# Kernel tuning notes

Hardware: AMD Instinct MI355X
Metric: run time of the kernel (lower is better)

The kernel has to match this reference:

```python
import jax, jax.numpy as jnp
import numpy as np


def _hard_sigmoid(x):
    # Keras ConvLSTM2D default recurrent_activation
    return jnp.clip(0.2 * x + 0.5, 0.0, 1.0)


def _conv(x, w):
    # NHWC input, HWIO kernel, SAME padding, stride 1
    return jax.lax.conv_general_dilated(
        x, w, (1, 1), 'SAME', dimension_numbers=('NHWC', 'HWIO', 'NHWC'))


def _convlstm(seq, h, c, k, rk, b):
    # seq: [B, T, H, W, Cin]; h, c: [B, H, W, F]
    # k: [kh, kw, Cin, 4F], rk: [kh, kw, F, 4F], b: [4F]
    def step(carry, x):
        h, c = carry
        z = _conv(x, k) + _conv(h, rk) + b  # [B,H,W,4F]
        zi, zf, zc, zo = jnp.split(z, 4, axis=-1)
        i = _hard_sigmoid(zi)
        f = _hard_sigmoid(zf)
        o = _hard_sigmoid(zo)
        c = f * c + i * jnp.tanh(zc)
        h = o * jnp.tanh(c)
        return (h, c), None
    (h, c), _ = jax.lax.scan(step, (h, c), jnp.swapaxes(seq, 0, 1))
    return h, c


def setup_inputs() -> dict:
    key = jax.random.key(0)
    ks = jax.random.split(key, 14)
    B, T, H, W, Cin, F, K = 32, 1, 64, 64, 1, 64, 3
    s = 0.05
    inp = {
        'input_': jax.random.normal(ks[0], (B, T, H, W, Cin), jnp.float32),
        'h0': jax.random.normal(ks[1], (B, H, W, F), jnp.float32) * s,
        'c0': jax.random.normal(ks[2], (B, H, W, F), jnp.float32) * s,
        'h1': jax.random.normal(ks[3], (B, H, W, F), jnp.float32) * s,
        'c1': jax.random.normal(ks[4], (B, H, W, F), jnp.float32) * s,
        'k0': jax.random.normal(ks[5], (K, K, Cin, 4 * F), jnp.float32) * s,
        'rk0': jax.random.normal(ks[6], (K, K, F, 4 * F), jnp.float32) * s,
        'b0': jnp.zeros((4 * F,), jnp.float32),
        'k1': jax.random.normal(ks[7], (K, K, F, 4 * F), jnp.float32) * s,
        'rk1': jax.random.normal(ks[8], (K, K, F, 4 * F), jnp.float32) * s,
        'b1': jnp.zeros((4 * F,), jnp.float32),
        'cw': jax.random.normal(ks[9], (1, 1, F, 1), jnp.float32) * s,
        'cb': jnp.zeros((1,), jnp.float32),
    }
    return inp


def reference(input_, h0, c0, h1, c1, k0, rk0, b0, k1, rk1, b1, cw, cb):
    # Layer 0 consumes the input frame sequence (T=1)
    h0n, c0n = _convlstm(input_, h0, c0, k0, rk0, b0)
    # Layer 1 consumes layer-0's last hidden state as its (length-1) input
    h1n, c1n = _convlstm(h0n[:, None], h1, c1, k1, rk1, b1)
    frames = _conv(h1n, cw) + cb  # 1x1 conv head -> [B,H,W,1]
    return frames, h0n, c0n, h1n, c1n
```

## Files before the change

kernel.cpp:

```cpp
#include <hip/hip_runtime.h>
#include <hip/hip_bf16.h>

typedef short s16;
typedef __attribute__((ext_vector_type(8))) short bf16x8;
typedef __attribute__((ext_vector_type(4))) float f32x4;

__device__ __forceinline__ s16 f2bf(float f) {
  unsigned u = __builtin_bit_cast(unsigned, f);
  unsigned r = (u + 0x7FFFu + ((u >> 16) & 1u)) >> 16;
  return (s16)r;
}

__device__ __forceinline__ float hsig(float x) {
  return fminf(fmaxf(0.2f * x + 0.5f, 0.0f), 1.0f);
}

#define PXS 66
#define ROWSZ (PXS * 64)
#define ASZ4 (4 * ROWSZ)

__global__ void wprep_kernel(const float* __restrict__ rk0, const float* __restrict__ k1,
                             const float* __restrict__ rk1, const float* __restrict__ k0,
                             s16* __restrict__ w0q, s16* __restrict__ w1q,
                             s16* __restrict__ w2q, s16* __restrict__ k0t) {
  int idx = blockIdx.x * 256 + threadIdx.x;
  const int n1 = 18 * 8192;
  if (idx < 3 * n1) {
    int which = idx / n1;
    int i = idx - which * n1;
    int e    = i & 7;
    int lane = (i >> 3) & 63;
    int g    = (i >> 9) & 3;
    int j    = (i >> 11) & 3;
    int k    = (i >> 13) & 1;
    int tap  = i >> 14;
    int l15 = lane & 15, l4 = lane >> 4;
    int ic = k * 32 + l4 * 8 + e;
    int oc = j * 64 + g * 16 + l15;
    const float* src = (which == 0) ? rk0 : (which == 1) ? k1 : rk1;
    s16* dst = (which == 0) ? w0q : (which == 1) ? w1q : w2q;
    dst[i] = f2bf(src[(tap * 64 + ic) * 256 + oc]);
  } else if (idx < 3 * n1 + 8192) {
    int r = idx - 3 * n1;
    int kk = r & 31;
    int oc = r >> 5;
    k0t[r] = (kk < 9) ? f2bf(k0[kk * 256 + oc]) : (s16)0;
  }
}

template <bool F32>
__device__ __forceinline__ bf16x8 load_conv8(const void* src, long off) {
  if constexpr (F32) {
    const float* p = (const float*)src + off;
    float4 v0 = *reinterpret_cast<const float4*>(p);
    float4 v1 = *reinterpret_cast<const float4*>(p + 4);
    bf16x8 r;
    r[0] = f2bf(v0.x); r[1] = f2bf(v0.y); r[2] = f2bf(v0.z); r[3] = f2bf(v0.w);
    r[4] = f2bf(v1.x); r[5] = f2bf(v1.y); r[6] = f2bf(v1.z); r[7] = f2bf(v1.w);
    return r;
  } else {
    return *reinterpret_cast<const bf16x8*>((const s16*)src + off);
  }
}

template <bool F32>
__device__ __forceinline__ void stage4(s16* a_lds, const void* src, int b, int y0, int tid) {
  #pragma unroll
  for (int i = 0; i < 2; ++i) {
    int c   = tid + i * 1024;
    int row = c >> 9;
    int px  = (c >> 3) & 63;
    int cb  = c & 7;
    int y   = y0 - 1 + row;
    int xp  = px + 1;
    bf16x8 v = {};
    if ((unsigned)y < 64u)
      v = load_conv8<F32>(src, ((long)(b * 64 + y) * 64 + px) * 64 + cb * 8);
    *reinterpret_cast<bf16x8*>(a_lds + (row * PXS + xp) * 64 + ((cb ^ (xp & 7)) * 8)) = v;
  }
  if (tid < 64) {
    int row = tid >> 4;
    int xp  = ((tid >> 3) & 1) ? 65 : 0;
    int cb  = tid & 7;
    bf16x8 z = {};
    *reinterpret_cast<bf16x8*>(a_lds + (row * PXS + xp) * 64 + cb * 8) = z;
  }
}

template <int NSRC, bool XPATH, bool S0F32, bool S1F32>
__global__ __launch_bounds__(1024, 4) void cell_kernel(
    const void* __restrict__ src0,
    const void* __restrict__ src1,
    const s16* __restrict__ w0,
    const s16* __restrict__ w1,
    const float* __restrict__ xin,
    const s16* __restrict__ k0t,
    const float* __restrict__ bias,
    const float* __restrict__ c_old,
    float* __restrict__ h_out,
    float* __restrict__ c_out,
    s16* __restrict__ hb_out)
{
  __shared__ __align__(16) s16 a_lds[NSRC * ASZ4];
  __shared__ __align__(16) s16 w_lds[4][8192];
  __shared__ float x_lds[XPATH ? 256 : 1];

  const int tid = threadIdx.x;
  const int b  = blockIdx.x >> 5;
  const int y0 = (blockIdx.x & 31) << 1;

  const int wave = tid >> 6;
  const int lane = tid & 63;
  const int g    = wave & 3;
  const int mq   = wave >> 2;
  const int l15  = lane & 15;
  const int l4   = lane >> 4;

  constexpr int NST = NSRC * 18;

  auto issueW = [&](int u) {
    int v = (u >= NST) ? u - NST : u;
    int si = (NSRC == 2 && v >= 18) ? 1 : 0;
    int vv = v - 18 * si;
    const s16* wt = (si ? w1 : w0) + vv * 8192;
    char* base = (char*)(&w_lds[0][0]) + (u & 3) * 16384 + (tid >> 6) * 1024;
    __builtin_amdgcn_global_load_lds(
        (const __attribute__((address_space(1))) void*)(wt + tid * 8),
        (__attribute__((address_space(3))) void*)base, 16, 0, 0);
  };

  auto readWf = [&](bf16x8 (&wf)[4], int u) {
    const s16* wb = &w_lds[u & 3][0] + g * 512 + lane * 8;
    #pragma unroll
    for (int j = 0; j < 4; ++j)
      wf[j] = *reinterpret_cast<const bf16x8*>(wb + j * 2048);
  };

  auto readA = [&](bf16x8 (&af)[2], int u) {
    int v = (u >= NST) ? u - NST : u;
    int si = (NSRC == 2 && v >= 18) ? 1 : 0;
    int uu = v - 18 * si;
    int tap = uu >> 1, kk = uu & 1;
    int dy = tap / 3, dx = tap - dy * 3;
    const char* sb = (const char*)a_lds + si * (ASZ4 * 2) + ((mq >> 1) + dy) * (ROWSZ * 2);
    #pragma unroll
    for (int m = 0; m < 2; ++m) {
      int xq   = (mq & 1) * 32 + m * 16 + l15 + dx;
      int boff = xq * 128 + ((((kk << 2) | l4) ^ (xq & 7)) << 4);
      af[m] = *reinterpret_cast<const bf16x8*>(sb + boff);
    }
  };

  f32x4 acc[2][4] = {};

  auto doMfma = [&](const bf16x8 (&af)[2], const bf16x8 (&wf)[4]) {
    __builtin_amdgcn_s_setprio(1);
    #pragma unroll
    for (int m = 0; m < 2; ++m) {
      #pragma unroll
      for (int j = 0; j < 4; ++j)
        acc[m][j] = __builtin_amdgcn_mfma_f32_16x16x32_bf16(af[m], wf[j], acc[m][j], 0, 0, 0);
    }
    __builtin_amdgcn_s_setprio(0);
  };

  issueW(0);
  issueW(1);
  issueW(2);
  stage4<S0F32>(a_lds, src0, b, y0, tid);
  if (NSRC == 2) stage4<S1F32>(a_lds + ASZ4, src1, b, y0, tid);
  if (XPATH) {
    if (tid < 256) {
      int row = tid >> 6, px = tid & 63;
      int y = y0 - 1 + row;
      x_lds[tid] = ((unsigned)y < 64u) ? xin[(b * 64 + y) * 64 + px] : 0.0f;
    }
  }
  __syncthreads();

  if (XPATH) {
    const int rb = mq >> 1;
    #pragma unroll
    for (int m = 0; m < 2; ++m) {
      int px = (mq & 1) * 32 + m * 16 + l15;
      bf16x8 ax = {};
      #pragma unroll
      for (int e = 0; e < 8; ++e) {
        int t = l4 * 8 + e;
        if (t < 9) {
          int dyt = t / 3, dxt = t - dyt * 3;
          int xx = px + dxt - 1;
          float xv = ((unsigned)xx < 64u) ? x_lds[(rb + dyt) * 64 + xx] : 0.0f;
          ax[e] = f2bf(xv);
        }
      }
      #pragma unroll
      for (int j = 0; j < 4; ++j) {
        int oc = j * 64 + g * 16 + l15;
        bf16x8 bx = *reinterpret_cast<const bf16x8*>(k0t + oc * 32 + l4 * 8);
        acc[m][j] = __builtin_amdgcn_mfma_f32_16x16x32_bf16(ax, bx, acc[m][j], 0, 0, 0);
      }
    }
  }

  bf16x8 afA[2], afB[2], wfA[4], wfB[4];
  readA(afA, 0);
  readWf(wfA, 0);
  #pragma unroll
  for (int u = 0; u < NST; u += 2) {
    asm volatile("s_waitcnt vmcnt(1)" ::: "memory");
    __builtin_amdgcn_s_barrier();
    issueW(u + 3);
    readA(afB, u + 1);
    readWf(wfB, u + 1);
    doMfma(afA, wfA);
    asm volatile("s_waitcnt vmcnt(1)" ::: "memory");
    __builtin_amdgcn_s_barrier();
    issueW(u + 4);
    readA(afA, u + 2);
    readWf(wfA, u + 2);
    doMfma(afB, wfB);
  }

  float bi[4];
  #pragma unroll
  for (int j = 0; j < 4; ++j) bi[j] = bias[j * 64 + g * 16 + l15];

  const int pix_base = b * 4096 + y0 * 64;
  const int f = g * 16 + l15;
  #pragma unroll
  for (int m = 0; m < 2; ++m) {
    #pragma unroll
    for (int r = 0; r < 4; ++r) {
      int pl = mq * 32 + m * 16 + l4 * 4 + r;
      int off = (pix_base + pl) * 64 + f;
      float zi = acc[m][0][r] + bi[0];
      float zf = acc[m][1][r] + bi[1];
      float zc = acc[m][2][r] + bi[2];
      float zo = acc[m][3][r] + bi[3];
      float ig = hsig(zi), fg = hsig(zf), og = hsig(zo);
      float cn = fg * c_old[off] + ig * tanhf(zc);
      float hn = og * tanhf(cn);
      c_out[off] = cn;
      h_out[off] = hn;
      if (hb_out) hb_out[off] = f2bf(hn);
    }
  }
}

__global__ void frames_kernel(const float* __restrict__ h, const float* __restrict__ cw,
                              const float* __restrict__ cbp, float* __restrict__ out) {
  int tid = blockIdx.x * 256 + threadIdx.x;
  int p  = tid >> 2;
  int fc = (tid & 3) * 16;
  const float4* hp = reinterpret_cast<const float4*>(h + p * 64 + fc);
  const float4* wp = reinterpret_cast<const float4*>(cw + fc);
  float s = 0.0f;
  #pragma unroll
  for (int i = 0; i < 4; ++i) {
    float4 v = hp[i];
    float4 w = wp[i];
    s += v.x * w.x + v.y * w.y + v.z * w.z + v.w * w.w;
  }
  s += __shfl_xor(s, 1);
  s += __shfl_xor(s, 2);
  if ((tid & 3) == 0) out[p] = s + cbp[0];
}

extern "C" void kernel_launch(void* const* d_in, const int* in_sizes, int n_in,
                              void* d_out, int out_size, void* d_ws, size_t ws_size,
                              hipStream_t stream) {
  const float* x   = (const float*)d_in[0];
  const float* h0  = (const float*)d_in[1];
  const float* c0  = (const float*)d_in[2];
  const float* h1  = (const float*)d_in[3];
  const float* c1  = (const float*)d_in[4];
  const float* k0  = (const float*)d_in[5];
  const float* rk0 = (const float*)d_in[6];
  const float* b0  = (const float*)d_in[7];
  const float* k1  = (const float*)d_in[8];
  const float* rk1 = (const float*)d_in[9];
  const float* b1  = (const float*)d_in[10];
  const float* cw  = (const float*)d_in[11];
  const float* cbp = (const float*)d_in[12];

  float* out    = (float*)d_out;
  float* frames = out;
  float* h0n    = out + 131072;
  float* c0n    = out + 131072 + 8388608;
  float* h1n    = out + 131072 + 2 * 8388608;
  float* c1n    = out + 131072 + 3 * 8388608;

  char* ws = (char*)d_ws;
  const size_t SZ_H = 16777216;
  s16* h0nb = (s16*)(ws + 0 * SZ_H);
  s16* w0q  = (s16*)(ws + 1 * SZ_H);
  s16* w1q  = (s16*)(ws + 1 * SZ_H + 1 * 294912);
  s16* w2q  = (s16*)(ws + 1 * SZ_H + 2 * 294912);
  s16* k0t  = (s16*)(ws + 1 * SZ_H + 3 * 294912);

  wprep_kernel<<<1760, 256, 0, stream>>>(rk0, k1, rk1, k0, w0q, w1q, w2q, k0t);

  cell_kernel<1, true, true, false><<<1024, 1024, 0, stream>>>(
      h0, nullptr, w0q, nullptr, x, k0t, b0, c0, h0n, c0n, h0nb);

  cell_kernel<2, false, false, true><<<1024, 1024, 0, stream>>>(
      h0nb, h1, w1q, w2q, nullptr, nullptr, b1, c1, h1n, c1n, nullptr);

  frames_kernel<<<2048, 256, 0, stream>>>(h1n, cw, cbp, frames);
}
```

Before: 188.8 us.

## Retile layer-1 cell kernel to 4 rows per block with larger per-wave tiles

```diff
diff --git a/kernel.cpp b/kernel.cpp
--- a/kernel.cpp
+++ b/kernel.cpp
@@ -18,6 +18,7 @@
 #define PXS 66
 #define ROWSZ (PXS * 64)
 #define ASZ4 (4 * ROWSZ)
+#define ASZ6 (6 * ROWSZ)
 
 __global__ void wprep_kernel(const float* __restrict__ rk0, const float* __restrict__ k1,
                              const float* __restrict__ rk1, const float* __restrict__ k0,
@@ -63,11 +64,11 @@
   }
 }
 
-template <bool F32>
-__device__ __forceinline__ void stage4(s16* a_lds, const void* src, int b, int y0, int tid) {
-  #pragma unroll
-  for (int i = 0; i < 2; ++i) {
-    int c   = tid + i * 1024;
+template <bool F32, int ROWS, int NT>
+__device__ __forceinline__ void stageA(s16* a_lds, const void* src, int b, int y0, int tid) {
+  #pragma unroll
+  for (int i = 0; i < ROWS * 512 / NT; ++i) {
+    int c   = tid + i * NT;
     int row = c >> 9;
     int px  = (c >> 3) & 63;
     int cb  = c & 7;
@@ -78,7 +79,7 @@
       v = load_conv8<F32>(src, ((long)(b * 64 + y) * 64 + px) * 64 + cb * 8);
     *reinterpret_cast<bf16x8*>(a_lds + (row * PXS + xp) * 64 + ((cb ^ (xp & 7)) * 8)) = v;
   }
-  if (tid < 64) {
+  if (tid < ROWS * 16) {
     int row = tid >> 4;
     int xp  = ((tid >> 3) & 1) ? 65 : 0;
     int cb  = tid & 7;
@@ -87,12 +88,9 @@
   }
 }
 
-template <int NSRC, bool XPATH, bool S0F32, bool S1F32>
-__global__ __launch_bounds__(1024, 4) void cell_kernel(
-    const void* __restrict__ src0,
-    const void* __restrict__ src1,
+__global__ __launch_bounds__(1024, 4) void cell0_kernel(
+    const float* __restrict__ h0,
     const s16* __restrict__ w0,
-    const s16* __restrict__ w1,
     const float* __restrict__ xin,
     const s16* __restrict__ k0t,
     const float* __restrict__ bias,
@@ -101,9 +99,9 @@
     float* __restrict__ c_out,
     s16* __restrict__ hb_out)
 {
-  __shared__ __align__(16) s16 a_lds[NSRC * ASZ4];
+  __shared__ __align__(16) s16 a_lds[ASZ4];
   __shared__ __align__(16) s16 w_lds[4][8192];
-  __shared__ float x_lds[XPATH ? 256 : 1];
+  __shared__ float x_lds[256];
 
   const int tid = threadIdx.x;
   const int b  = blockIdx.x >> 5;
@@ -116,33 +114,27 @@
   const int l15  = lane & 15;
   const int l4   = lane >> 4;
 
-  constexpr int NST = NSRC * 18;
+  constexpr int NST = 18;
 
   auto issueW = [&](int u) {
     int v = (u >= NST) ? u - NST : u;
-    int si = (NSRC == 2 && v >= 18) ? 1 : 0;
-    int vv = v - 18 * si;
-    const s16* wt = (si ? w1 : w0) + vv * 8192;
+    const s16* wt = w0 + v * 8192;
     char* base = (char*)(&w_lds[0][0]) + (u & 3) * 16384 + (tid >> 6) * 1024;
     __builtin_amdgcn_global_load_lds(
         (const __attribute__((address_space(1))) void*)(wt + tid * 8),
         (__attribute__((address_space(3))) void*)base, 16, 0, 0);
   };
-
   auto readWf = [&](bf16x8 (&wf)[4], int u) {
     const s16* wb = &w_lds[u & 3][0] + g * 512 + lane * 8;
     #pragma unroll
     for (int j = 0; j < 4; ++j)
       wf[j] = *reinterpret_cast<const bf16x8*>(wb + j * 2048);
   };
-
   auto readA = [&](bf16x8 (&af)[2], int u) {
     int v = (u >= NST) ? u - NST : u;
-    int si = (NSRC == 2 && v >= 18) ? 1 : 0;
-    int uu = v - 18 * si;
-    int tap = uu >> 1, kk = uu & 1;
+    int tap = v >> 1, kk = v & 1;
     int dy = tap / 3, dx = tap - dy * 3;
-    const char* sb = (const char*)a_lds + si * (ASZ4 * 2) + ((mq >> 1) + dy) * (ROWSZ * 2);
+    const char* sb = (const char*)a_lds + ((mq >> 1) + dy) * (ROWSZ * 2);
     #pragma unroll
     for (int m = 0; m < 2; ++m) {
       int xq   = (mq & 1) * 32 + m * 16 + l15 + dx;
@@ -167,18 +159,15 @@
   issueW(0);
   issueW(1);
   issueW(2);
-  stage4<S0F32>(a_lds, src0, b, y0, tid);
-  if (NSRC == 2) stage4<S1F32>(a_lds + ASZ4, src1, b, y0, tid);
-  if (XPATH) {
-    if (tid < 256) {
-      int row = tid >> 6, px = tid & 63;
-      int y = y0 - 1 + row;
-      x_lds[tid] = ((unsigned)y < 64u) ? xin[(b * 64 + y) * 64 + px] : 0.0f;
-    }
+  stageA<true, 4, 1024>(a_lds, h0, b, y0, tid);
+  if (tid < 256) {
+    int row = tid >> 6, px = tid & 63;
+    int y = y0 - 1 + row;
+    x_lds[tid] = ((unsigned)y < 64u) ? xin[(b * 64 + y) * 64 + px] : 0.0f;
   }
   __syncthreads();
 
-  if (XPATH) {
+  {
     const int rb = mq >> 1;
     #pragma unroll
     for (int m = 0; m < 2; ++m) {
@@ -225,7 +214,6 @@
   float bi[4];
   #pragma unroll
   for (int j = 0; j < 4; ++j) bi[j] = bias[j * 64 + g * 16 + l15];
-
   const int pix_base = b * 4096 + y0 * 64;
   const int f = g * 16 + l15;
   #pragma unroll
@@ -243,7 +231,125 @@
       float hn = og * tanhf(cn);
       c_out[off] = cn;
       h_out[off] = hn;
-      if (hb_out) hb_out[off] = f2bf(hn);
+      hb_out[off] = f2bf(hn);
+    }
+  }
+}
+
+__global__ __launch_bounds__(512, 2) void cell1_kernel(
+    const s16* __restrict__ src0,
+    const float* __restrict__ src1,
+    const s16* __restrict__ w0,
+    const s16* __restrict__ w1,
+    const float* __restrict__ bias,
+    const float* __restrict__ c_old,
+    float* __restrict__ h_out,
+    float* __restrict__ c_out)
+{
+  __shared__ __align__(16) s16 a_lds[2 * ASZ6];
+  __shared__ __align__(16) s16 w_lds[3][8192];
+
+  const int tid = threadIdx.x;
+  const int b  = blockIdx.x >> 4;
+  const int y0 = (blockIdx.x & 15) << 2;
+
+  const int wave = tid >> 6;
+  const int lane = tid & 63;
+  const int g    = wave & 3;
+  const int mh   = wave >> 2;
+  const int l15  = lane & 15;
+  const int l4   = lane >> 4;
+
+  constexpr int NST = 36;
+
+  auto issueW = [&](int u) {
+    int v = (u >= NST) ? u - NST : u;
+    int si = (v >= 18) ? 1 : 0;
+    const s16* wt = (si ? w1 : w0) + (v - 18 * si) * 8192;
+    char* sl = (char*)(&w_lds[0][0]) + (u % 3) * 16384 + wave * 1024;
+    __builtin_amdgcn_global_load_lds(
+        (const __attribute__((address_space(1))) void*)(wt + wave * 512 + lane * 8),
+        (__attribute__((address_space(3))) void*)sl, 16, 0, 0);
+    __builtin_amdgcn_global_load_lds(
+        (const __attribute__((address_space(1))) void*)(wt + 4096 + wave * 512 + lane * 8),
+        (__attribute__((address_space(3))) void*)(sl + 8192), 16, 0, 0);
+  };
+
+  auto readWf = [&](bf16x8 (&wf)[4], int u) {
+    const s16* wb = &w_lds[0][0] + (u % 3) * 8192 + g * 512 + lane * 8;
+    #pragma unroll
+    for (int j = 0; j < 4; ++j)
+      wf[j] = *reinterpret_cast<const bf16x8*>(wb + j * 2048);
+  };
+
+  f32x4 acc[8][4] = {};
+
+  auto doStage = [&](const bf16x8 (&wf)[4], int u) {
+    int si = (u >= 18) ? 1 : 0;
+    int uu = u - 18 * si;
+    int tap = uu >> 1, kk = uu & 1;
+    int dy = tap / 3, dx = tap - dy * 3;
+    const char* sb = (const char*)a_lds + si * (ASZ6 * 2);
+    bf16x8 af[8];
+    #pragma unroll
+    for (int m = 0; m < 8; ++m) {
+      int row  = 2 * mh + (m >> 2) + dy;
+      int xq   = (m & 3) * 16 + l15 + dx;
+      int boff = xq * 128 + ((((kk << 2) | l4) ^ (xq & 7)) << 4);
+      af[m] = *reinterpret_cast<const bf16x8*>(sb + row * (ROWSZ * 2) + boff);
+    }
+    __builtin_amdgcn_s_setprio(1);
+    #pragma unroll
+    for (int m = 0; m < 8; ++m) {
+      #pragma unroll
+      for (int j = 0; j < 4; ++j)
+        acc[m][j] = __builtin_amdgcn_mfma_f32_16x16x32_bf16(af[m], wf[j], acc[m][j], 0, 0, 0);
+    }
+    __builtin_amdgcn_s_setprio(0);
+  };
+
+  issueW(0);
+  issueW(1);
+  stageA<false, 6, 512>(a_lds, src0, b, y0, tid);
+  stageA<true, 6, 512>(a_lds + ASZ6, src1, b, y0, tid);
+  __syncthreads();
+
+  bf16x8 wfA[4], wfB[4];
+  readWf(wfA, 0);
+  #pragma unroll
+  for (int u = 0; u < NST; u += 2) {
+    asm volatile("s_waitcnt vmcnt(0)" ::: "memory");
+    __builtin_amdgcn_s_barrier();
+    issueW(u + 2);
+    readWf(wfB, u + 1);
+    doStage(wfA, u);
+    asm volatile("s_waitcnt vmcnt(0)" ::: "memory");
+    __builtin_amdgcn_s_barrier();
+    issueW(u + 3);
+    readWf(wfA, (u + 2 < NST) ? u + 2 : 0);
+    doStage(wfB, u + 1);
+  }
+
+  float bi[4];
+  #pragma unroll
+  for (int j = 0; j < 4; ++j) bi[j] = bias[j * 64 + g * 16 + l15];
+  const int pix_base = b * 4096 + y0 * 64;
+  const int f = g * 16 + l15;
+  #pragma unroll
+  for (int m = 0; m < 8; ++m) {
+    #pragma unroll
+    for (int r = 0; r < 4; ++r) {
+      int pl = (2 * mh + (m >> 2)) * 64 + (m & 3) * 16 + l4 * 4 + r;
+      int off = (pix_base + pl) * 64 + f;
+      float zi = acc[m][0][r] + bi[0];
+      float zf = acc[m][1][r] + bi[1];
+      float zc = acc[m][2][r] + bi[2];
+      float zo = acc[m][3][r] + bi[3];
+      float ig = hsig(zi), fg = hsig(zf), og = hsig(zo);
+      float cn = fg * c_old[off] + ig * tanhf(zc);
+      float hn = og * tanhf(cn);
+      c_out[off] = cn;
+      h_out[off] = hn;
     }
   }
 }
@@ -301,11 +407,11 @@
 
   wprep_kernel<<<1760, 256, 0, stream>>>(rk0, k1, rk1, k0, w0q, w1q, w2q, k0t);
 
-  cell_kernel<1, true, true, false><<<1024, 1024, 0, stream>>>(
-      h0, nullptr, w0q, nullptr, x, k0t, b0, c0, h0n, c0n, h0nb);
-
-  cell_kernel<2, false, false, true><<<1024, 1024, 0, stream>>>(
-      h0nb, h1, w1q, w2q, nullptr, nullptr, b1, c1, h1n, c1n, nullptr);
+  cell0_kernel<<<1024, 1024, 0, stream>>>(
+      h0, w0q, x, k0t, b0, c0, h0n, c0n, h0nb);
+
+  cell1_kernel<<<512, 512, 0, stream>>>(
+      h0nb, h1, w1q, w2q, b1, c1, h1n, c1n);
 
   frames_kernel<<<2048, 256, 0, stream>>>(h1n, cw, cbp, frames);
 }
```

Result: slower. 202.6 us (+7.3%).
